# Kernel optimization log

Measured on AMD Instinct MI355X. Metric: run time of the kernel, lower is better.

Reference implementation:

```python
import jax, jax.numpy as jnp
import numpy as np

HS, WS = 8, 8          # window size (idx=0, split_size=[8,8])
NH = 6                 # num_heads
DIM = 192
HEAD_DIM = DIM // NH
SCALE = HEAD_DIM ** -0.5
POS_DIM = (DIM // 4) // 4  # = 12


def _rpe_biases_np():
    bh = np.arange(1 - HS, HS)
    bw = np.arange(1 - WS, WS)
    b = np.stack(np.meshgrid(bh, bw, indexing='ij'))  # (2, 2HS-1, 2WS-1)
    return b.reshape(2, -1).T.astype(np.float32)      # (M, 2)


def _rel_index_np():
    coords = np.stack(np.meshgrid(np.arange(HS), np.arange(WS), indexing='ij'))
    cf = coords.reshape(2, -1)                        # (2, N)
    rel = (cf[:, :, None] - cf[:, None, :]).transpose(1, 2, 0)  # (N, N, 2)
    rel[:, :, 0] += HS - 1
    rel[:, :, 1] += WS - 1
    rel[:, :, 0] *= 2 * WS - 1
    return rel.sum(-1)                                # (N, N) int


def _ln(x, g, b):
    m = jnp.mean(x, -1, keepdims=True)
    v = jnp.var(x, -1, keepdims=True)
    return (x - m) / jnp.sqrt(v + 1e-5) * g + b


def setup_inputs() -> dict:
    key = jax.random.key(0)
    ks = jax.random.split(key, 8)
    B, H, W = 4, 256, 256
    L = H * W
    d = {
        'q': jax.random.normal(ks[0], (B, L, DIM), jnp.float32),
        'k': jax.random.normal(ks[1], (B, L, DIM), jnp.float32),
        'v': jax.random.normal(ks[2], (B, L, DIM), jnp.float32),
        'H': H,
        'W': W,
        'w_proj': jax.random.normal(ks[3], (2, POS_DIM), jnp.float32) * 0.1,
        'b_proj': jnp.zeros((POS_DIM,), jnp.float32),
        'ln1_g': jnp.ones((POS_DIM,), jnp.float32),
        'ln1_b': jnp.zeros((POS_DIM,), jnp.float32),
        'w1': jax.random.normal(ks[4], (POS_DIM, POS_DIM), jnp.float32) * 0.1,
        'b1': jnp.zeros((POS_DIM,), jnp.float32),
        'ln2_g': jnp.ones((POS_DIM,), jnp.float32),
        'ln2_b': jnp.zeros((POS_DIM,), jnp.float32),
        'w2': jax.random.normal(ks[5], (POS_DIM, POS_DIM), jnp.float32) * 0.1,
        'b2': jnp.zeros((POS_DIM,), jnp.float32),
        'ln3_g': jnp.ones((POS_DIM,), jnp.float32),
        'ln3_b': jnp.zeros((POS_DIM,), jnp.float32),
        'w3': jax.random.normal(ks[6], (POS_DIM, NH), jnp.float32) * 0.1,
        'b3': jnp.zeros((NH,), jnp.float32),
    }
    return d


def reference(q, k, v, H, W, w_proj, b_proj, ln1_g, ln1_b, w1, b1,
              ln2_g, ln2_b, w2, b2, ln3_g, ln3_b, w3, b3):
    B, L, C = q.shape
    N = HS * WS

    def im2win(x):
        # (B, L, C) -> (B*nW, NH, N, head_dim)
        x = x.reshape(B, H // HS, HS, W // WS, WS, C)
        x = x.transpose(0, 1, 3, 2, 4, 5).reshape(-1, N, NH, C // NH)
        return x.transpose(0, 2, 1, 3)

    qw = im2win(q) * SCALE
    kw = im2win(k)
    vw = im2win(v)

    attn = jnp.einsum('whnd,whmd->whnm', qw, kw)  # (B*nW, NH, N, N)

    # dynamic relative position bias MLP
    biases = jnp.asarray(_rpe_biases_np())        # (M, 2)
    rel_idx = jnp.asarray(_rel_index_np())        # (N, N)
    pos = biases @ w_proj + b_proj
    pos = jax.nn.relu(_ln(pos, ln1_g, ln1_b)) @ w1 + b1
    pos = jax.nn.relu(_ln(pos, ln2_g, ln2_b)) @ w2 + b2
    pos = jax.nn.relu(_ln(pos, ln3_g, ln3_b)) @ w3 + b3  # (M, NH)
    rpb = pos[rel_idx.reshape(-1)].reshape(N, N, NH).transpose(2, 0, 1)  # (NH, N, N)

    attn = jax.nn.softmax(attn + rpb[None], axis=-1)
    out = jnp.einsum('whnm,whmd->whnd', attn, vw)  # (B*nW, NH, N, hd)
    out = out.transpose(0, 2, 1, 3).reshape(-1, N, C)
    # windows2img -> (B, H, W, C)
    out = out.reshape(B, H // HS, W // WS, HS, WS, C)
    out = out.transpose(0, 1, 3, 2, 4, 5).reshape(B, H, W, C)
    return out
```

## Files before the change

### kernel.cpp

```cpp
#include <hip/hip_runtime.h>


#define NTOK  64
#define NHEAD 6
#define HD    32
#define CDIM  192
#define POSD  12
#define MROWS 225
#define SCALE 0.17677669529663687f

__device__ __forceinline__ void ln_relu(const float* x, float* r,
                                        const float* __restrict__ g,
                                        const float* __restrict__ b) {
  float mean = 0.f;
#pragma unroll
  for (int j = 0; j < POSD; ++j) mean += x[j];
  mean *= (1.0f / POSD);
  float var = 0.f;
#pragma unroll
  for (int j = 0; j < POSD; ++j) { float d = x[j] - mean; var += d * d; }
  var *= (1.0f / POSD);
  const float rstd = rsqrtf(var + 1e-5f);
#pragma unroll
  for (int j = 0; j < POSD; ++j) {
    float t = (x[j] - mean) * rstd * g[j] + b[j];
    r[j] = t > 0.f ? t : 0.f;
  }
}

__global__ __launch_bounds__(256) void rpe_mlp_kernel(
    const float* __restrict__ w_proj, const float* __restrict__ b_proj,
    const float* __restrict__ ln1_g, const float* __restrict__ ln1_b,
    const float* __restrict__ w1,    const float* __restrict__ b1,
    const float* __restrict__ ln2_g, const float* __restrict__ ln2_b,
    const float* __restrict__ w2,    const float* __restrict__ b2,
    const float* __restrict__ ln3_g, const float* __restrict__ ln3_b,
    const float* __restrict__ w3,    const float* __restrict__ b3,
    float* __restrict__ rpb)
{
  __shared__ float pos_s[MROWS * NHEAD];
  const int m = threadIdx.x;
  if (m < MROWS) {
    const float bh = (float)(m / 15 - 7);
    const float bw = (float)(m % 15 - 7);
    float x[POSD], r[POSD];
#pragma unroll
    for (int j = 0; j < POSD; ++j)
      x[j] = bh * w_proj[j] + bw * w_proj[POSD + j] + b_proj[j];

    ln_relu(x, r, ln1_g, ln1_b);
#pragma unroll
    for (int j = 0; j < POSD; ++j) {
      float a = b1[j];
#pragma unroll
      for (int kk = 0; kk < POSD; ++kk) a += r[kk] * w1[kk * POSD + j];
      x[j] = a;
    }
    ln_relu(x, r, ln2_g, ln2_b);
#pragma unroll
    for (int j = 0; j < POSD; ++j) {
      float a = b2[j];
#pragma unroll
      for (int kk = 0; kk < POSD; ++kk) a += r[kk] * w2[kk * POSD + j];
      x[j] = a;
    }
    ln_relu(x, r, ln3_g, ln3_b);
#pragma unroll
    for (int hh = 0; hh < NHEAD; ++hh) {
      float a = b3[hh];
#pragma unroll
      for (int kk = 0; kk < POSD; ++kk) a += r[kk] * w3[kk * NHEAD + hh];
      pos_s[m * NHEAD + hh] = a;
    }
  }
  __syncthreads();
  for (int idx = threadIdx.x; idx < NHEAD * NTOK * NTOK; idx += blockDim.x) {
    const int h = idx >> 12;
    const int r = idx & 4095;
    const int i = r >> 6, j = r & 63;
    const int dy = (i >> 3) - (j >> 3) + 7;
    const int dx = (i & 7) - (j & 7) + 7;
    rpb[idx] = pos_s[(dy * 15 + dx) * NHEAD + h];
  }
}

__global__ __launch_bounds__(64) void attn_kernel(
    const float* __restrict__ q, const float* __restrict__ k,
    const float* __restrict__ v, const float* __restrict__ rpb,
    float* __restrict__ out)
{
  __shared__ float Ks[NTOK * HD];
  __shared__ float Vs[NTOK * HD];

  const int w  = blockIdx.x;
  const int h  = blockIdx.y;
  const int b  = w >> 10;
  const int wy = (w >> 5) & 31;
  const int wx = w & 31;
  const int tid = threadIdx.x;

  const int gbase = ((b * 256 + wy * 8) * 256 + wx * 8) * CDIM + h * HD;

  {
    const int vec = tid & 7;
#pragma unroll
    for (int p = 0; p < 8; ++p) {
      const int r  = p * 8 + (tid >> 3);
      const int go = gbase + ((r >> 3) * 256 + (r & 7)) * CDIM + vec * 4;
      float4 kk = *(const float4*)(k + go);
      float4 vv = *(const float4*)(v + go);
      ((float4*)Ks)[r * 8 + vec] = kk;
      ((float4*)Vs)[r * 8 + vec] = vv;
    }
  }

  float qreg[HD];
  {
    const int go = gbase + ((tid >> 3) * 256 + (tid & 7)) * CDIM;
#pragma unroll
    for (int t = 0; t < 8; ++t) {
      float4 f = *(const float4*)(q + go + t * 4);
      qreg[4 * t + 0] = f.x * SCALE;
      qreg[4 * t + 1] = f.y * SCALE;
      qreg[4 * t + 2] = f.z * SCALE;
      qreg[4 * t + 3] = f.w * SCALE;
    }
  }

  float s[NTOK];
  {
    const float4* rp4 = (const float4*)(rpb + h * (NTOK * NTOK) + tid * NTOK);
#pragma unroll
    for (int t = 0; t < 16; ++t) {
      float4 f = rp4[t];
      s[4 * t + 0] = f.x; s[4 * t + 1] = f.y;
      s[4 * t + 2] = f.z; s[4 * t + 3] = f.w;
    }
  }

  __syncthreads();

  const float4* Ks4 = (const float4*)Ks;
#pragma unroll
  for (int j = 0; j < NTOK; ++j) {
    float acc = 0.f;
#pragma unroll
    for (int d = 0; d < 8; ++d) {
      float4 kk = Ks4[j * 8 + d];
      acc += qreg[4 * d + 0] * kk.x + qreg[4 * d + 1] * kk.y +
             qreg[4 * d + 2] * kk.z + qreg[4 * d + 3] * kk.w;
    }
    s[j] += acc;
  }

  float mx = s[0];
#pragma unroll
  for (int j = 1; j < NTOK; ++j) mx = fmaxf(mx, s[j]);
  float sum = 0.f;
#pragma unroll
  for (int j = 0; j < NTOK; ++j) {
    float e = __expf(s[j] - mx);
    s[j] = e;
    sum += e;
  }
  const float inv = 1.0f / sum;

  float o[HD];
#pragma unroll
  for (int d = 0; d < HD; ++d) o[d] = 0.f;
  const float4* Vs4 = (const float4*)Vs;
#pragma unroll
  for (int j = 0; j < NTOK; ++j) {
    const float p = s[j];
#pragma unroll
    for (int d = 0; d < 8; ++d) {
      float4 vv = Vs4[j * 8 + d];
      o[4 * d + 0] += p * vv.x;
      o[4 * d + 1] += p * vv.y;
      o[4 * d + 2] += p * vv.z;
      o[4 * d + 3] += p * vv.w;
    }
  }

  {
    const int go = gbase + ((tid >> 3) * 256 + (tid & 7)) * CDIM;
#pragma unroll
    for (int t = 0; t < 8; ++t) {
      float4 f = make_float4(o[4 * t + 0] * inv, o[4 * t + 1] * inv,
                             o[4 * t + 2] * inv, o[4 * t + 3] * inv);
      *(float4*)(out + go + t * 4) = f;
    }
  }
}

extern "C" void kernel_launch(void* const* d_in, const int* in_sizes, int n_in,
                              void* d_out, int out_size, void* d_ws, size_t ws_size,
                              hipStream_t stream)
{
  const float* q      = (const float*)d_in[0];
  const float* k      = (const float*)d_in[1];
  const float* v      = (const float*)d_in[2];
  const float* w_proj = (const float*)d_in[5];
  const float* b_proj = (const float*)d_in[6];
  const float* ln1_g  = (const float*)d_in[7];
  const float* ln1_b  = (const float*)d_in[8];
  const float* w1     = (const float*)d_in[9];
  const float* b1     = (const float*)d_in[10];
  const float* ln2_g  = (const float*)d_in[11];
  const float* ln2_b  = (const float*)d_in[12];
  const float* w2     = (const float*)d_in[13];
  const float* b2     = (const float*)d_in[14];
  const float* ln3_g  = (const float*)d_in[15];
  const float* ln3_b  = (const float*)d_in[16];
  const float* w3     = (const float*)d_in[17];
  const float* b3     = (const float*)d_in[18];
  float* out = (float*)d_out;
  float* rpb = (float*)d_ws;

  const int B = in_sizes[0] / (256 * 256 * CDIM);

  rpe_mlp_kernel<<<1, 256, 0, stream>>>(w_proj, b_proj, ln1_g, ln1_b, w1, b1,
                                        ln2_g, ln2_b, w2, b2, ln3_g, ln3_b,
                                        w3, b3, rpb);

  dim3 grid(B * 1024, NHEAD);
  attn_kernel<<<grid, 64, 0, stream>>>(q, k, v, rpb, out);
}
```

Baseline: 731.3 us.

## Rewrite window attention with bf16 MFMA and one block per window

New measurement: 610.7 us. 16.5% less time.

```diff
diff --git a/kernel.cpp b/kernel.cpp
--- a/kernel.cpp
+++ b/kernel.cpp
@@ -1,13 +1,25 @@
 #include <hip/hip_runtime.h>
 
 
-#define NTOK  64
 #define NHEAD 6
-#define HD    32
 #define CDIM  192
 #define POSD  12
-#define MROWS 225
 #define SCALE 0.17677669529663687f
+#define PSTRIDE 152
+
+typedef __attribute__((ext_vector_type(8))) short short8;
+typedef __attribute__((ext_vector_type(4))) short short4v;
+typedef __attribute__((ext_vector_type(4))) float f32x4;
+
+__device__ __forceinline__ short f2bf(float f) {
+  unsigned u = __float_as_uint(f);
+  u = (u + 0x7FFFu + ((u >> 16) & 1u)) >> 16;
+  return (short)u;
+}
+
+__device__ __forceinline__ int tokoff(int t) {
+  return ((t >> 3) * 256 + (t & 7)) * CDIM;
+}
 
 __device__ __forceinline__ void ln_relu(const float* x, float* r,
                                         const float* __restrict__ g,
@@ -36,18 +48,17 @@
     const float* __restrict__ w2,    const float* __restrict__ b2,
     const float* __restrict__ ln3_g, const float* __restrict__ ln3_b,
     const float* __restrict__ w3,    const float* __restrict__ b3,
-    float* __restrict__ rpb)
+    float* __restrict__ rpb_sw)
 {
-  __shared__ float pos_s[MROWS * NHEAD];
+  __shared__ float pos_s[225 * NHEAD];
   const int m = threadIdx.x;
-  if (m < MROWS) {
+  if (m < 225) {
     const float bh = (float)(m / 15 - 7);
     const float bw = (float)(m % 15 - 7);
     float x[POSD], r[POSD];
 #pragma unroll
     for (int j = 0; j < POSD; ++j)
       x[j] = bh * w_proj[j] + bw * w_proj[POSD + j] + b_proj[j];
-
     ln_relu(x, r, ln1_g, ln1_b);
 #pragma unroll
     for (int j = 0; j < POSD; ++j) {
@@ -74,122 +85,144 @@
     }
   }
   __syncthreads();
-  for (int idx = threadIdx.x; idx < NHEAD * NTOK * NTOK; idx += blockDim.x) {
-    const int h = idx >> 12;
-    const int r = idx & 4095;
-    const int i = r >> 6, j = r & 63;
-    const int dy = (i >> 3) - (j >> 3) + 7;
-    const int dx = (i & 7) - (j & 7) + 7;
-    rpb[idx] = pos_s[(dy * 15 + dx) * NHEAD + h];
-  }
-}
-
-__global__ __launch_bounds__(64) void attn_kernel(
+
+  const int base = blockIdx.x * 256 + threadIdx.x;
+  const int lane = base & 63;
+  const int qt = (base >> 6) & 3;
+  const int km = (base >> 8) & 3;
+  const int h  = base >> 10;
+  const int c = lane & 15, qq = lane >> 4;
+  const int query = 16 * qt + c;
+  f32x4 vv;
+#pragma unroll
+  for (int r = 0; r < 4; ++r) {
+    const int key = 16 * km + 4 * qq + r;
+    const int dy = (query >> 3) - (key >> 3) + 7;
+    const int dx = (query & 7) - (key & 7) + 7;
+    vv[r] = pos_s[(dy * 15 + dx) * NHEAD + h];
+  }
+  *(f32x4*)(rpb_sw + base * 4) = vv;
+}
+
+__global__ __launch_bounds__(384) void attn_kernel(
     const float* __restrict__ q, const float* __restrict__ k,
-    const float* __restrict__ v, const float* __restrict__ rpb,
+    const float* __restrict__ v, const float* __restrict__ rpb_sw,
     float* __restrict__ out)
 {
-  __shared__ float Ks[NTOK * HD];
-  __shared__ float Vs[NTOK * HD];
+  __shared__ char Pall[NHEAD * 64 * PSTRIDE];
+  const int wv   = threadIdx.x >> 6;
+  const int lane = threadIdx.x & 63;
+  const int c = lane & 15, qq = lane >> 4;
+  char* Pb = Pall + wv * (64 * PSTRIDE);
 
   const int w  = blockIdx.x;
-  const int h  = blockIdx.y;
-  const int b  = w >> 10;
-  const int wy = (w >> 5) & 31;
-  const int wx = w & 31;
-  const int tid = threadIdx.x;
-
-  const int gbase = ((b * 256 + wy * 8) * 256 + wx * 8) * CDIM + h * HD;
-
-  {
-    const int vec = tid & 7;
-#pragma unroll
-    for (int p = 0; p < 8; ++p) {
-      const int r  = p * 8 + (tid >> 3);
-      const int go = gbase + ((r >> 3) * 256 + (r & 7)) * CDIM + vec * 4;
-      float4 kk = *(const float4*)(k + go);
-      float4 vv = *(const float4*)(v + go);
-      ((float4*)Ks)[r * 8 + vec] = kk;
-      ((float4*)Vs)[r * 8 + vec] = vv;
-    }
-  }
-
-  float qreg[HD];
-  {
-    const int go = gbase + ((tid >> 3) * 256 + (tid & 7)) * CDIM;
-#pragma unroll
-    for (int t = 0; t < 8; ++t) {
-      float4 f = *(const float4*)(q + go + t * 4);
-      qreg[4 * t + 0] = f.x * SCALE;
-      qreg[4 * t + 1] = f.y * SCALE;
-      qreg[4 * t + 2] = f.z * SCALE;
-      qreg[4 * t + 3] = f.w * SCALE;
-    }
-  }
-
-  float s[NTOK];
-  {
-    const float4* rp4 = (const float4*)(rpb + h * (NTOK * NTOK) + tid * NTOK);
-#pragma unroll
-    for (int t = 0; t < 16; ++t) {
-      float4 f = rp4[t];
-      s[4 * t + 0] = f.x; s[4 * t + 1] = f.y;
-      s[4 * t + 2] = f.z; s[4 * t + 3] = f.w;
-    }
-  }
-
-  __syncthreads();
-
-  const float4* Ks4 = (const float4*)Ks;
-#pragma unroll
-  for (int j = 0; j < NTOK; ++j) {
-    float acc = 0.f;
-#pragma unroll
-    for (int d = 0; d < 8; ++d) {
-      float4 kk = Ks4[j * 8 + d];
-      acc += qreg[4 * d + 0] * kk.x + qreg[4 * d + 1] * kk.y +
-             qreg[4 * d + 2] * kk.z + qreg[4 * d + 3] * kk.w;
-    }
-    s[j] += acc;
-  }
-
-  float mx = s[0];
-#pragma unroll
-  for (int j = 1; j < NTOK; ++j) mx = fmaxf(mx, s[j]);
-  float sum = 0.f;
-#pragma unroll
-  for (int j = 0; j < NTOK; ++j) {
-    float e = __expf(s[j] - mx);
-    s[j] = e;
-    sum += e;
-  }
-  const float inv = 1.0f / sum;
-
-  float o[HD];
-#pragma unroll
-  for (int d = 0; d < HD; ++d) o[d] = 0.f;
-  const float4* Vs4 = (const float4*)Vs;
-#pragma unroll
-  for (int j = 0; j < NTOK; ++j) {
-    const float p = s[j];
-#pragma unroll
-    for (int d = 0; d < 8; ++d) {
-      float4 vv = Vs4[j * 8 + d];
-      o[4 * d + 0] += p * vv.x;
-      o[4 * d + 1] += p * vv.y;
-      o[4 * d + 2] += p * vv.z;
-      o[4 * d + 3] += p * vv.w;
-    }
-  }
-
-  {
-    const int go = gbase + ((tid >> 3) * 256 + (tid & 7)) * CDIM;
-#pragma unroll
-    for (int t = 0; t < 8; ++t) {
-      float4 f = make_float4(o[4 * t + 0] * inv, o[4 * t + 1] * inv,
-                             o[4 * t + 2] * inv, o[4 * t + 3] * inv);
-      *(float4*)(out + go + t * 4) = f;
-    }
+  const int b  = w >> 10, wy = (w >> 5) & 31, wx = w & 31;
+  const int gbase = ((b * 256 + wy * 8) * 256 + wx * 8) * CDIM + wv * 32;
+
+  short8 ka[4], qb[4];
+#pragma unroll
+  for (int t = 0; t < 4; ++t) {
+    const int go = gbase + tokoff(16 * t + c) + 8 * qq;
+    f32x4 k0 = *(const f32x4*)(k + go), k1 = *(const f32x4*)(k + go + 4);
+    f32x4 q0 = *(const f32x4*)(q + go), q1 = *(const f32x4*)(q + go + 4);
+#pragma unroll
+    for (int j = 0; j < 4; ++j) {
+      ka[t][j]     = f2bf(k0[j]);
+      ka[t][4 + j] = f2bf(k1[j]);
+      qb[t][j]     = f2bf(q0[j] * SCALE);
+      qb[t][4 + j] = f2bf(q1[j] * SCALE);
+    }
+  }
+
+  short8 va[2][2];
+#pragma unroll
+  for (int ks = 0; ks < 2; ++ks)
+#pragma unroll
+    for (int mt = 0; mt < 2; ++mt) {
+      short8 f;
+#pragma unroll
+      for (int j = 0; j < 8; ++j)
+        f[j] = f2bf(v[gbase + tokoff(8 * qq + j + 32 * ks) + 16 * mt + c]);
+      va[mt][ks] = f;
+    }
+
+  f32x4 acc[4][4];
+#pragma unroll
+  for (int km = 0; km < 4; ++km)
+#pragma unroll
+    for (int qt = 0; qt < 4; ++qt)
+      acc[km][qt] = *((const f32x4*)rpb_sw + (wv * 16 + km * 4 + qt) * 64 + lane);
+#pragma unroll
+  for (int km = 0; km < 4; ++km)
+#pragma unroll
+    for (int qt = 0; qt < 4; ++qt)
+      acc[km][qt] = __builtin_amdgcn_mfma_f32_16x16x32_bf16(
+          ka[km], qb[qt], acc[km][qt], 0, 0, 0);
+
+#pragma unroll
+  for (int qt = 0; qt < 4; ++qt) {
+    float mx = acc[0][qt][0];
+#pragma unroll
+    for (int km = 0; km < 4; ++km)
+#pragma unroll
+      for (int r = 0; r < 4; ++r) mx = fmaxf(mx, acc[km][qt][r]);
+    mx = fmaxf(mx, __shfl_xor(mx, 16, 64));
+    mx = fmaxf(mx, __shfl_xor(mx, 32, 64));
+    float sm = 0.f;
+#pragma unroll
+    for (int km = 0; km < 4; ++km)
+#pragma unroll
+      for (int r = 0; r < 4; ++r) {
+        float e = __expf(acc[km][qt][r] - mx);
+        acc[km][qt][r] = e;
+        sm += e;
+      }
+    sm += __shfl_xor(sm, 16, 64);
+    sm += __shfl_xor(sm, 32, 64);
+    const float inv = 1.0f / sm;
+#pragma unroll
+    for (int km = 0; km < 4; ++km)
+#pragma unroll
+      for (int r = 0; r < 4; ++r) acc[km][qt][r] *= inv;
+  }
+
+#pragma unroll
+  for (int km = 0; km < 4; ++km)
+#pragma unroll
+    for (int qt = 0; qt < 4; ++qt) {
+      short4v pk;
+#pragma unroll
+      for (int r = 0; r < 4; ++r) pk[r] = f2bf(acc[km][qt][r]);
+      *(short4v*)(Pb + (16 * qt + c) * PSTRIDE + (16 * km + 4 * qq) * 2) = pk;
+    }
+
+  f32x4 o[2][4];
+#pragma unroll
+  for (int mt = 0; mt < 2; ++mt)
+#pragma unroll
+    for (int nt = 0; nt < 4; ++nt) o[mt][nt] = (f32x4){0.f, 0.f, 0.f, 0.f};
+#pragma unroll
+  for (int ks = 0; ks < 2; ++ks)
+#pragma unroll
+    for (int nt = 0; nt < 4; ++nt) {
+      const char* rp = Pb + (16 * nt + c) * PSTRIDE + 16 * qq + 64 * ks;
+      short4v p0 = *(const short4v*)rp;
+      short4v p1 = *(const short4v*)(rp + 8);
+      short8 pb;
+#pragma unroll
+      for (int j = 0; j < 4; ++j) { pb[j] = p0[j]; pb[4 + j] = p1[j]; }
+#pragma unroll
+      for (int mt = 0; mt < 2; ++mt)
+        o[mt][nt] = __builtin_amdgcn_mfma_f32_16x16x32_bf16(
+            va[mt][ks], pb, o[mt][nt], 0, 0, 0);
+    }
+
+#pragma unroll
+  for (int nt = 0; nt < 4; ++nt) {
+    const int go = gbase + tokoff(16 * nt + c) + 4 * qq;
+#pragma unroll
+    for (int mt = 0; mt < 2; ++mt)
+      *(f32x4*)(out + go + 16 * mt) = o[mt][nt];
   }
 }
 
@@ -215,14 +248,13 @@
   const float* w3     = (const float*)d_in[17];
   const float* b3     = (const float*)d_in[18];
   float* out = (float*)d_out;
-  float* rpb = (float*)d_ws;
+  float* rpb_sw = (float*)d_ws;
 
   const int B = in_sizes[0] / (256 * 256 * CDIM);
 
-  rpe_mlp_kernel<<<1, 256, 0, stream>>>(w_proj, b_proj, ln1_g, ln1_b, w1, b1,
-                                        ln2_g, ln2_b, w2, b2, ln3_g, ln3_b,
-                                        w3, b3, rpb);
-
-  dim3 grid(B * 1024, NHEAD);
-  attn_kernel<<<grid, 64, 0, stream>>>(q, k, v, rpb, out);
-}
+  rpe_mlp_kernel<<<24, 256, 0, stream>>>(w_proj, b_proj, ln1_g, ln1_b, w1, b1,
+                                         ln2_g, ln2_b, w2, b2, ln3_g, ln3_b,
+                                         w3, b3, rpb_sw);
+
+  attn_kernel<<<B * 1024, 384, 0, stream>>>(q, k, v, rpb_sw, out);
+}
```
